# Kernel optimization log

Measured on AMD Instinct MI355X. Metric: run time of the kernel, lower is better.

Reference implementation:

```python
import jax, jax.numpy as jnp
import numpy as np

NUM_EMBEDDINGS = 512
EMBEDDING_DIM = 64
COMMITMENT_COST = 0.25


def setup_inputs() -> dict:
    key = jax.random.key(0)
    k1, k2 = jax.random.split(key)
    z = jax.random.normal(k1, (32, 4096, EMBEDDING_DIM), dtype=jnp.float32)
    # original init: uniform(-1/K, 1/K)
    emb_w = (jax.random.uniform(k2, (NUM_EMBEDDINGS, EMBEDDING_DIM), dtype=jnp.float32) * 2.0 - 1.0) / NUM_EMBEDDINGS
    return {"z": z, "emb_w": emb_w}


def reference(z, emb_w):
    # z: [B, T, D]; emb_w: [K, D]
    input_shape = z.shape
    flat_z = z.reshape(-1, EMBEDDING_DIM)  # [N, D]
    # squared L2 distances: [N, K]
    distances = (jnp.sum(flat_z ** 2, axis=1, keepdims=True)
                 + jnp.sum(emb_w ** 2, axis=1)
                 - 2.0 * flat_z @ emb_w.T)
    encoding_indices = jnp.argmin(distances, axis=1)  # [N]
    # direct gather instead of one-hot matmul (same math)
    quantized = emb_w[encoding_indices].reshape(input_shape)

    e_latent_loss = jnp.mean((jax.lax.stop_gradient(quantized) - z) ** 2)
    q_latent_loss = jnp.mean((quantized - jax.lax.stop_gradient(z)) ** 2)
    loss = q_latent_loss + COMMITMENT_COST * e_latent_loss

    # straight-through estimator
    quantized_st = z + jax.lax.stop_gradient(quantized - z)

    # perplexity from code usage histogram (== mean of one-hot rows)
    n_tokens = flat_z.shape[0]
    counts = jnp.zeros((NUM_EMBEDDINGS,), dtype=jnp.float32).at[encoding_indices].add(1.0)
    avg_probs = counts / n_tokens
    perplexity = jnp.exp(-jnp.sum(avg_probs * jnp.log(avg_probs + 1e-10)))

    min_distance = jnp.min(distances, axis=1).mean()
    encodings = encoding_indices.reshape(input_shape[:-1])
    return quantized_st, loss, perplexity, encodings, min_distance
```

## Files before the change

kernel.cpp:

```cpp
#include <hip/hip_runtime.h>
#include <math.h>

#define D 64
#define K 512
#define N_TOK (32 * 4096)
#define SBLK 512
#define TPB 256
#define EPS 4e-5f
#define BFLAG 64

#define Q_OFF    0
#define LOSS_OFF 8388608
#define PERP_OFF 8388609
#define ENC_OFF  8388610
#define MIND_OFF 8519682


typedef __attribute__((ext_vector_type(8))) short  short8;
typedef __attribute__((ext_vector_type(4))) float  f32x4;

__device__ __forceinline__ short f2bf(float x) {
    unsigned u = __builtin_bit_cast(unsigned, x);
    unsigned r = (u + 0x7fffu + ((u >> 16) & 1u)) >> 16;
    return (short)r;
}
__device__ __forceinline__ float bf2f(short s) {
    unsigned u = ((unsigned)(unsigned short)s) << 16;
    return __builtin_bit_cast(float, u);
}
__device__ __forceinline__ f32x4 mfma16(short8 a, short8 b, f32x4 c) {
    return __builtin_amdgcn_mfma_f32_16x16x32_bf16(a, b, c, 0, 0, 0);
}

__device__ __forceinline__ float np_sumsq64(const float* x) {
    float r[8];
    #pragma unroll
    for (int j = 0; j < 8; ++j) r[j] = __fmul_rn(x[j], x[j]);
    #pragma unroll
    for (int i = 8; i < 64; i += 8) {
        #pragma unroll
        for (int j = 0; j < 8; ++j)
            r[j] = __fadd_rn(r[j], __fmul_rn(x[i + j], x[i + j]));
    }
    float l = __fadd_rn(__fadd_rn(r[0], r[1]), __fadd_rn(r[2], r[3]));
    float h = __fadd_rn(__fadd_rn(r[4], r[5]), __fadd_rn(r[6], r[7]));
    return __fadd_rn(l, h);
}

__global__ __launch_bounds__(256) void vq_prep(const float* __restrict__ ew,
                                               float* __restrict__ wsf,
                                               short* __restrict__ img) {
    int gt = blockIdx.x * 256 + threadIdx.x;
    int c = gt >> 9, s = gt & 511;
    int grp = s >> 6, l = s & 63;
    int plane = grp >> 2, f = (grp >> 1) & 1, sub = grp & 1;
    int k  = c * 32 + sub * 16 + (l & 15);
    int d0 = f * 32 + (l >> 4) * 8;
    const float* p = ew + (size_t)k * D + d0;
    short8 v;
    #pragma unroll
    for (int j = 0; j < 8; ++j) {
        float x = p[j];
        short hs = f2bf(x);
        v[j] = plane ? f2bf(__fsub_rn(x, bf2f(hs))) : hs;
    }
    *(short8*)(img + (size_t)gt * 8) = v;

    if (gt < 516) wsf[512 + gt] = 0.0f;

    if (gt < K) {
        float row[D];
        const float* q = ew + (size_t)gt * D;
        #pragma unroll
        for (int d = 0; d < D; ++d) row[d] = q[d];
        wsf[gt] = np_sumsq64(row);
    }
}

__global__ __launch_bounds__(SBLK, 4) void vq_screen(
    const float* __restrict__ z, const float* __restrict__ ew,
    const short* __restrict__ img, const float* __restrict__ b2,
    float* __restrict__ out, float* __restrict__ S, int* __restrict__ gcnt)
{
    __shared__ __align__(16) short lbuf[16384];
    __shared__ float s_mhb2[K];
    __shared__ int   s_cnt[K];
    __shared__ float s_zrow[8][D];
    __shared__ int   s_flag[BFLAG];
    __shared__ int   s_nf;

    const int tid  = threadIdx.x;
    const int lane = tid & 63;
    const int wid  = tid >> 6;
    const int col  = lane & 15, g = lane >> 4;
    const int tbase = blockIdx.x * TPB + wid * 32;

    if (tid == 0) s_nf = 0;
    s_cnt[tid]  = 0;
    s_mhb2[tid] = -0.5f * b2[tid];

#define STAGE_QTR(s) do {                                                    \
        _Pragma("unroll")                                                    \
        for (int i_ = 0; i_ < 4; ++i_) {                                     \
            int idx_ = i_ * SBLK + tid;                   \
            short8 v_ = *(const short8*)(img + ((size_t)(s) * 2048 + idx_) * 8); \
            *(short8*)&lbuf[(size_t)idx_ * 8] = v_;                          \
        }                                                                    \
    } while (0)

    STAGE_QTR(0);

    short8 zhi[2][2], zlo[2][2];
    float zss = 0.f;
    #pragma unroll
    for (int t = 0; t < 2; ++t) {
        const f32x4* zr = (const f32x4*)(z + (size_t)(tbase + t * 16 + col) * D);
        #pragma unroll
        for (int f = 0; f < 2; ++f) {
            f32x4 va = zr[f * 8 + g * 2], vb = zr[f * 8 + g * 2 + 1];
            float v[8] = {va[0], va[1], va[2], va[3], vb[0], vb[1], vb[2], vb[3]};
            short8 h8, l8;
            #pragma unroll
            for (int j = 0; j < 8; ++j) {
                float x = v[j];
                short hs = f2bf(x);
                h8[j] = hs;
                l8[j] = f2bf(__fsub_rn(x, bf2f(hs)));
                zss = fmaf(x, x, zss);
            }
            zhi[t][f] = h8; zlo[t][f] = l8;
        }
    }

    float best[2][4], sec[2][4];
    int   kk[2][4];
    #pragma unroll
    for (int t = 0; t < 2; ++t)
        #pragma unroll
        for (int r = 0; r < 4; ++r) { best[t][r] = -1e30f; sec[t][r] = -1e30f; kk[t][r] = 0; }

#define COMPUTE_QTR(s) do {                                                  \
        _Pragma("unroll 2")                                                  \
        for (int j_ = 0; j_ < 4; ++j_) {                                     \
            const short* bp_ = &lbuf[(j_ * 512 + lane) * 8];                 \
            _Pragma("unroll")                                                \
            for (int sub_ = 0; sub_ < 2; ++sub_) {                           \
                short8 ah0_ = *(const short8*)(bp_ + (0 + sub_) * 512);      \
                short8 ah1_ = *(const short8*)(bp_ + (2 + sub_) * 512);      \
                short8 al0_ = *(const short8*)(bp_ + (4 + sub_) * 512);      \
                short8 al1_ = *(const short8*)(bp_ + (6 + sub_) * 512);      \
                const int c0_ = ((s) * 4 + j_) * 32 + sub_ * 16 + g * 4;     \
                f32x4 mhb_ = *(const f32x4*)&s_mhb2[c0_];                    \
                _Pragma("unroll")                                            \
                for (int t_ = 0; t_ < 2; ++t_) {                             \
                    f32x4 a1_ = mhb_;                \
                    f32x4 a2_ = (f32x4){0.f, 0.f, 0.f, 0.f};      \
                    a1_ = mfma16(ah0_, zhi[t_][0], a1_);                     \
                    a2_ = mfma16(ah1_, zhi[t_][1], a2_);                     \
                    a1_ = mfma16(ah0_, zlo[t_][0], a1_);                     \
                    a2_ = mfma16(ah1_, zlo[t_][1], a2_);                     \
                    a1_ = mfma16(al0_, zhi[t_][0], a1_);                     \
                    a2_ = mfma16(al1_, zhi[t_][1], a2_);                     \
                    _Pragma("unroll")                                        \
                    for (int r_ = 0; r_ < 4; ++r_) {                         \
                        float sc_ = a1_[r_] + a2_[r_];                       \
                        bool  g_  = sc_ > best[t_][r_];                      \
                                \
                        sec[t_][r_]  = fmaxf(fminf(sc_, best[t_][r_]),       \
                                             sec[t_][r_]);                   \
                        best[t_][r_] = fmaxf(best[t_][r_], sc_);             \
                        kk[t_][r_]   = g_ ? c0_ + r_ : kk[t_][r_];           \
                    }                                                        \
                }                                                            \
            }                                                                \
        }                                                                    \
    } while (0)

    __syncthreads();
    COMPUTE_QTR(0);
    #pragma unroll 1
    for (int s = 1; s < 4; ++s) {
        __syncthreads();
        STAGE_QTR(s);
        __syncthreads();
        COMPUTE_QTR(s);
    }
#undef STAGE_QTR
#undef COMPUTE_QTR

    float b1[2], b2s[2];
    int   k1[2];
#define MERGE2(bx, sx, kx, by, sy, ky, bo, so, ko) do {                      \
        if ((by) > (bx)) { bo = (by); so = fmaxf((bx), (sy)); ko = (ky); }   \
        else             { bo = (bx); so = fmaxf((by), (sx)); ko = (kx); }   \
    } while (0)
    #pragma unroll
    for (int t = 0; t < 2; ++t) {
        float bA, sA, bB, sB; int kA, kB;
        MERGE2(best[t][0], sec[t][0], kk[t][0], best[t][1], sec[t][1], kk[t][1], bA, sA, kA);
        MERGE2(best[t][2], sec[t][2], kk[t][2], best[t][3], sec[t][3], kk[t][3], bB, sB, kB);
        MERGE2(bA, sA, kA, bB, sB, kB, b1[t], b2s[t], k1[t]);
    }
#undef MERGE2

    #pragma unroll
    for (int t = 0; t < 2; ++t) {
        #pragma unroll
        for (int m = 16; m < 64; m <<= 1) {
            float ob = __shfl_xor(b1[t], m);
            float os = __shfl_xor(b2s[t], m);
            int   ok = __shfl_xor(k1[t], m);
            if (ob > b1[t])       { b2s[t] = fmaxf(b1[t], os); b1[t] = ob; k1[t] = ok; }
            else if (ob == b1[t]) { b2s[t] = b1[t]; if (ok < k1[t]) k1[t] = ok; }
            else                  { b2s[t] = fmaxf(b2s[t], ob); }
        }
    }

    if (lane < 16) {
        #pragma unroll
        for (int t = 0; t < 2; ++t) {
            const int tok = tbase + t * 16 + col;
            out[ENC_OFF + tok] = (float)k1[t];
            atomicAdd(&s_cnt[k1[t]], 1);
            if (b1[t] - b2s[t] < EPS) {
                int slot = atomicAdd(&s_nf, 1);
                if (slot < BFLAG) s_flag[slot] = tok | (k1[t] << 17);
            }
        }
    }

    #pragma unroll
    for (int p = 0; p < 4; ++p) {
        const int tt   = p >> 1;
        const int cidx = (p & 1) * 8 + (lane >> 3);
        const int kq   = __shfl(k1[tt], cidx);
        const int tok  = tbase + tt * 16 + cidx;
        const int dc   = (lane & 7) * 8;
        const f32x4* zr4 = (const f32x4*)(z + (size_t)tok * D + dc);
        const f32x4* er4 = (const f32x4*)(ew + (size_t)kq * D + dc);
        f32x4 z0 = zr4[0], z1 = zr4[1], e0 = er4[0], e1 = er4[1], o0, o1;
        #pragma unroll
        for (int r = 0; r < 4; ++r) {
            o0[r] = __fadd_rn(z0[r], __fsub_rn(e0[r], z0[r]));
            o1[r] = __fadd_rn(z1[r], __fsub_rn(e1[r], z1[r]));
        }
        f32x4* op = (f32x4*)(out + Q_OFF + (size_t)tok * D + dc);
        op[0] = o0; op[1] = o1;
    }

    float contrib = zss + ((lane < 16) ? -2.f * (b1[0] + b1[1]) : 0.f);
    #pragma unroll
    for (int off = 32; off; off >>= 1) contrib += __shfl_down(contrib, off);
    if (lane == 0) atomicAdd(S, contrib);

    __syncthreads();
    int nf = s_nf; if (nf > BFLAG) nf = BFLAG;
    for (int fi = wid; fi < nf; fi += 8) {
        const int packed = s_flag[fi];
        const int tok    = packed & 0x1FFFF;
        const int oldk   = packed >> 17;

        s_zrow[wid][lane] = z[(size_t)tok * D + lane];
        const float an = np_sumsq64(&s_zrow[wid][0]);

        float bd = 1e30f; int bk = 0;
        #pragma unroll 1
        for (int j = 0; j < 8; ++j) {
            const int c = j * 64 + lane;
            const float* e0 = ew + (size_t)c * D;
            float gacc = 0.f;
            #pragma unroll
            for (int d = 0; d < D; ++d)
                gacc = fmaf(s_zrow[wid][d], e0[d], gacc);
            const float b2c = __fmul_rn(-2.f, s_mhb2[c]);
            float dd = fmaf(-2.f, gacc, __fadd_rn(an, b2c));
            if (dd < bd) { bd = dd; bk = c; }
        }
        #pragma unroll
        for (int off = 32; off; off >>= 1) {
            float obd = __shfl_down(bd, off);
            int   obk = __shfl_down(bk, off);
            if (obd < bd || (obd == bd && obk < bk)) { bd = obd; bk = obk; }
        }
        bk = __shfl(bk, 0);

        if (bk != oldk) {
            float zv = s_zrow[wid][lane];
            float ev = ew[(size_t)bk * D + lane];
            out[Q_OFF + (size_t)tok * D + lane] = __fadd_rn(zv, __fsub_rn(ev, zv));
            if (lane == 0) {
                out[ENC_OFF + tok] = (float)bk;
                atomicAdd(&s_cnt[bk], 1);
                atomicAdd(&s_cnt[oldk], -1);
            }
        }
    }

    __syncthreads();
    int cc = s_cnt[tid];
    if (cc) atomicAdd(&gcnt[tid], cc);
}

__global__ void vq_fin(const float* __restrict__ S, const int* __restrict__ gcnt,
                       float* __restrict__ out)
{
    __shared__ float red[8];
    int t = threadIdx.x;
    float p = (float)gcnt[t] * (1.f / (float)N_TOK);
    float term = p * logf(p + 1e-10f);
    #pragma unroll
    for (int off = 32; off; off >>= 1) term += __shfl_down(term, off);
    if ((t & 63) == 0) red[t >> 6] = term;
    __syncthreads();
    if (t == 0) {
        float s = 0.f;
        #pragma unroll
        for (int i = 0; i < 8; ++i) s += red[i];
        float Sv = S[0];
        out[PERP_OFF] = expf(-s);
        out[LOSS_OFF] = 1.25f * Sv * (1.f / (float)(N_TOK * D));
        out[MIND_OFF] = Sv * (1.f / (float)N_TOK);
    }
}

extern "C" void kernel_launch(void* const* d_in, const int* in_sizes, int n_in,
                              void* d_out, int out_size, void* d_ws, size_t ws_size,
                              hipStream_t stream)
{
    const float* z  = (const float*)d_in[0];
    const float* ew = (const float*)d_in[1];
    float* out = (float*)d_out;
    float* wsf = (float*)d_ws;

    float* Sp   = wsf + 512;
    int*   gcnt = (int*)(wsf + 514);
    short* img  = (short*)(wsf + 16384);

    vq_prep  <<<32, 256, 0, stream>>>(ew, wsf, img);
    vq_screen<<<N_TOK / TPB, SBLK, 0, stream>>>(z, ew, img, wsf, out, Sp, gcnt);
    vq_fin   <<<1, 512, 0, stream>>>(Sp, gcnt, out);
}
```

Before: 123.6 us.

## Halve tokens per block and double-buffer codebook staging with register prefetch

After: 218.8 us. +77.0%, slower.

```diff
diff --git a/kernel.cpp b/kernel.cpp
--- a/kernel.cpp
+++ b/kernel.cpp
@@ -5,7 +5,7 @@
 #define K 512
 #define N_TOK (32 * 4096)
 #define SBLK 512
-#define TPB 256
+#define TPB 128
 #define EPS 4e-5f
 #define BFLAG 64
 
@@ -77,12 +77,12 @@
     }
 }
 
-__global__ __launch_bounds__(SBLK, 4) void vq_screen(
+__global__ __launch_bounds__(SBLK, 6) void vq_screen(
     const float* __restrict__ z, const float* __restrict__ ew,
     const short* __restrict__ img, const float* __restrict__ b2,
     float* __restrict__ out, float* __restrict__ S, int* __restrict__ gcnt)
 {
-    __shared__ __align__(16) short lbuf[16384];
+    __shared__ __align__(16) short lbuf[2][4096];
     __shared__ float s_mhb2[K];
     __shared__ int   s_cnt[K];
     __shared__ float s_zrow[8][D];
@@ -93,28 +93,21 @@
     const int lane = tid & 63;
     const int wid  = tid >> 6;
     const int col  = lane & 15, g = lane >> 4;
-    const int tbase = blockIdx.x * TPB + wid * 32;
+    const int tbase = blockIdx.x * TPB + wid * 16;
 
     if (tid == 0) s_nf = 0;
     s_cnt[tid]  = 0;
     s_mhb2[tid] = -0.5f * b2[tid];
 
-#define STAGE_QTR(s) do {                                                    \
-        _Pragma("unroll")                                                    \
-        for (int i_ = 0; i_ < 4; ++i_) {                                     \
-            int idx_ = i_ * SBLK + tid;                   \
-            short8 v_ = *(const short8*)(img + ((size_t)(s) * 2048 + idx_) * 8); \
-            *(short8*)&lbuf[(size_t)idx_ * 8] = v_;                          \
-        }                                                                    \
-    } while (0)
-
-    STAGE_QTR(0);
-
-    short8 zhi[2][2], zlo[2][2];
+    {
+        short8 v = *(const short8*)(img + (size_t)tid * 8);
+        *(short8*)&lbuf[0][(size_t)tid * 8] = v;
+    }
+
+    short8 zhi[2], zlo[2];
     float zss = 0.f;
-    #pragma unroll
-    for (int t = 0; t < 2; ++t) {
-        const f32x4* zr = (const f32x4*)(z + (size_t)(tbase + t * 16 + col) * D);
+    {
+        const f32x4* zr = (const f32x4*)(z + (size_t)(tbase + col) * D);
         #pragma unroll
         for (int f = 0; f < 2; ++f) {
             f32x4 va = zr[f * 8 + g * 2], vb = zr[f * 8 + g * 2 + 1];
@@ -128,113 +121,92 @@
                 l8[j] = f2bf(__fsub_rn(x, bf2f(hs)));
                 zss = fmaf(x, x, zss);
             }
-            zhi[t][f] = h8; zlo[t][f] = l8;
-        }
-    }
-
-    float best[2][4], sec[2][4];
-    int   kk[2][4];
-    #pragma unroll
-    for (int t = 0; t < 2; ++t)
-        #pragma unroll
-        for (int r = 0; r < 4; ++r) { best[t][r] = -1e30f; sec[t][r] = -1e30f; kk[t][r] = 0; }
-
-#define COMPUTE_QTR(s) do {                                                  \
-        _Pragma("unroll 2")                                                  \
-        for (int j_ = 0; j_ < 4; ++j_) {                                     \
-            const short* bp_ = &lbuf[(j_ * 512 + lane) * 8];                 \
-            _Pragma("unroll")                                                \
-            for (int sub_ = 0; sub_ < 2; ++sub_) {                           \
-                short8 ah0_ = *(const short8*)(bp_ + (0 + sub_) * 512);      \
-                short8 ah1_ = *(const short8*)(bp_ + (2 + sub_) * 512);      \
-                short8 al0_ = *(const short8*)(bp_ + (4 + sub_) * 512);      \
-                short8 al1_ = *(const short8*)(bp_ + (6 + sub_) * 512);      \
-                const int c0_ = ((s) * 4 + j_) * 32 + sub_ * 16 + g * 4;     \
-                f32x4 mhb_ = *(const f32x4*)&s_mhb2[c0_];                    \
-                _Pragma("unroll")                                            \
-                for (int t_ = 0; t_ < 2; ++t_) {                             \
-                    f32x4 a1_ = mhb_;                \
-                    f32x4 a2_ = (f32x4){0.f, 0.f, 0.f, 0.f};      \
-                    a1_ = mfma16(ah0_, zhi[t_][0], a1_);                     \
-                    a2_ = mfma16(ah1_, zhi[t_][1], a2_);                     \
-                    a1_ = mfma16(ah0_, zlo[t_][0], a1_);                     \
-                    a2_ = mfma16(ah1_, zlo[t_][1], a2_);                     \
-                    a1_ = mfma16(al0_, zhi[t_][0], a1_);                     \
-                    a2_ = mfma16(al1_, zhi[t_][1], a2_);                     \
-                    _Pragma("unroll")                                        \
-                    for (int r_ = 0; r_ < 4; ++r_) {                         \
-                        float sc_ = a1_[r_] + a2_[r_];                       \
-                        bool  g_  = sc_ > best[t_][r_];                      \
-                                \
-                        sec[t_][r_]  = fmaxf(fminf(sc_, best[t_][r_]),       \
-                                             sec[t_][r_]);                   \
-                        best[t_][r_] = fmaxf(best[t_][r_], sc_);             \
-                        kk[t_][r_]   = g_ ? c0_ + r_ : kk[t_][r_];           \
-                    }                                                        \
-                }                                                            \
-            }                                                                \
-        }                                                                    \
-    } while (0)
+            zhi[f] = h8; zlo[f] = l8;
+        }
+    }
+
+    float best[4] = {-1e30f, -1e30f, -1e30f, -1e30f};
+    float sec[4]  = {-1e30f, -1e30f, -1e30f, -1e30f};
+    int   kk[4]   = {0, 0, 0, 0};
 
     __syncthreads();
-    COMPUTE_QTR(0);
-    #pragma unroll 1
-    for (int s = 1; s < 4; ++s) {
+
+    #pragma unroll 2
+    for (int c = 0; c < 16; ++c) {
+        short8 nxt;
+        if (c < 15)
+            nxt = *(const short8*)(img + ((size_t)(c + 1) * 512 + tid) * 8);
+
+        const short* bp = &lbuf[c & 1][lane * 8];
+        #pragma unroll
+        for (int sub = 0; sub < 2; ++sub) {
+            short8 ah0 = *(const short8*)(bp + (0 + sub) * 512);
+            short8 ah1 = *(const short8*)(bp + (2 + sub) * 512);
+            short8 al0 = *(const short8*)(bp + (4 + sub) * 512);
+            short8 al1 = *(const short8*)(bp + (6 + sub) * 512);
+            const int c0 = c * 32 + sub * 16 + g * 4;
+            f32x4 mhb = *(const f32x4*)&s_mhb2[c0];
+            f32x4 a1 = mhb;
+            f32x4 a2 = (f32x4){0.f, 0.f, 0.f, 0.f};
+            a1 = mfma16(ah0, zhi[0], a1);
+            a2 = mfma16(ah1, zhi[1], a2);
+            a1 = mfma16(ah0, zlo[0], a1);
+            a2 = mfma16(ah1, zlo[1], a2);
+            a1 = mfma16(al0, zhi[0], a1);
+            a2 = mfma16(al1, zhi[1], a2);
+            #pragma unroll
+            for (int r = 0; r < 4; ++r) {
+                float sc = a1[r] + a2[r];
+                bool  gg = sc > best[r];
+                sec[r]  = fmaxf(fminf(sc, best[r]), sec[r]);
+                best[r] = fmaxf(best[r], sc);
+                kk[r]   = gg ? c0 + r : kk[r];
+            }
+        }
+
+        if (c < 15)
+            *(short8*)&lbuf[(c + 1) & 1][(size_t)tid * 8] = nxt;
         __syncthreads();
-        STAGE_QTR(s);
-        __syncthreads();
-        COMPUTE_QTR(s);
-    }
-#undef STAGE_QTR
-#undef COMPUTE_QTR
-
-    float b1[2], b2s[2];
-    int   k1[2];
+    }
+
+    float b1, b2s; int k1;
 #define MERGE2(bx, sx, kx, by, sy, ky, bo, so, ko) do {                      \
         if ((by) > (bx)) { bo = (by); so = fmaxf((bx), (sy)); ko = (ky); }   \
         else             { bo = (bx); so = fmaxf((by), (sx)); ko = (kx); }   \
     } while (0)
-    #pragma unroll
-    for (int t = 0; t < 2; ++t) {
+    {
         float bA, sA, bB, sB; int kA, kB;
-        MERGE2(best[t][0], sec[t][0], kk[t][0], best[t][1], sec[t][1], kk[t][1], bA, sA, kA);
-        MERGE2(best[t][2], sec[t][2], kk[t][2], best[t][3], sec[t][3], kk[t][3], bB, sB, kB);
-        MERGE2(bA, sA, kA, bB, sB, kB, b1[t], b2s[t], k1[t]);
+        MERGE2(best[0], sec[0], kk[0], best[1], sec[1], kk[1], bA, sA, kA);
+        MERGE2(best[2], sec[2], kk[2], best[3], sec[3], kk[3], bB, sB, kB);
+        MERGE2(bA, sA, kA, bB, sB, kB, b1, b2s, k1);
     }
 #undef MERGE2
 
     #pragma unroll
-    for (int t = 0; t < 2; ++t) {
-        #pragma unroll
-        for (int m = 16; m < 64; m <<= 1) {
-            float ob = __shfl_xor(b1[t], m);
-            float os = __shfl_xor(b2s[t], m);
-            int   ok = __shfl_xor(k1[t], m);
-            if (ob > b1[t])       { b2s[t] = fmaxf(b1[t], os); b1[t] = ob; k1[t] = ok; }
-            else if (ob == b1[t]) { b2s[t] = b1[t]; if (ok < k1[t]) k1[t] = ok; }
-            else                  { b2s[t] = fmaxf(b2s[t], ob); }
-        }
+    for (int m = 16; m < 64; m <<= 1) {
+        float ob = __shfl_xor(b1, m);
+        float os = __shfl_xor(b2s, m);
+        int   ok = __shfl_xor(k1, m);
+        if (ob > b1)       { b2s = fmaxf(b1, os); b1 = ob; k1 = ok; }
+        else if (ob == b1) { b2s = b1; if (ok < k1) k1 = ok; }
+        else               { b2s = fmaxf(b2s, ob); }
     }
 
     if (lane < 16) {
-        #pragma unroll
-        for (int t = 0; t < 2; ++t) {
-            const int tok = tbase + t * 16 + col;
-            out[ENC_OFF + tok] = (float)k1[t];
-            atomicAdd(&s_cnt[k1[t]], 1);
-            if (b1[t] - b2s[t] < EPS) {
-                int slot = atomicAdd(&s_nf, 1);
-                if (slot < BFLAG) s_flag[slot] = tok | (k1[t] << 17);
-            }
-        }
-    }
-
-    #pragma unroll
-    for (int p = 0; p < 4; ++p) {
-        const int tt   = p >> 1;
-        const int cidx = (p & 1) * 8 + (lane >> 3);
-        const int kq   = __shfl(k1[tt], cidx);
-        const int tok  = tbase + tt * 16 + cidx;
+        const int tok = tbase + col;
+        out[ENC_OFF + tok] = (float)k1;
+        atomicAdd(&s_cnt[k1], 1);
+        if (b1 - b2s < EPS) {
+            int slot = atomicAdd(&s_nf, 1);
+            if (slot < BFLAG) s_flag[slot] = tok | (k1 << 17);
+        }
+    }
+
+    #pragma unroll
+    for (int p = 0; p < 2; ++p) {
+        const int cidx = p * 8 + (lane >> 3);
+        const int kq   = __shfl(k1, cidx);
+        const int tok  = tbase + cidx;
         const int dc   = (lane & 7) * 8;
         const f32x4* zr4 = (const f32x4*)(z + (size_t)tok * D + dc);
         const f32x4* er4 = (const f32x4*)(ew + (size_t)kq * D + dc);
@@ -248,7 +220,7 @@
         op[0] = o0; op[1] = o1;
     }
 
-    float contrib = zss + ((lane < 16) ? -2.f * (b1[0] + b1[1]) : 0.f);
+    float contrib = zss + ((lane < 16) ? -2.f * b1 : 0.f);
     #pragma unroll
     for (int off = 32; off; off >>= 1) contrib += __shfl_down(contrib, off);
     if (lane == 0) atomicAdd(S, contrib);
```
